# Kernel tuning notes

Hardware: AMD Instinct MI355X
Metric: run time of the kernel (lower is better)

Reference implementation:

```python
import jax, jax.numpy as jnp
import numpy as np

GAMMA = 0.9          # EMA momentum for prototype update
N_CLASSES = 201      # 200 classes + 1 background
K_PROTO = 5          # prototypes per class
FG_THRESH = 0.5      # pca_fg_threshold
SK_EPS = 0.05        # sinkhorn temperature (SwAV-style)
SK_ITERS = 3         # sinkhorn iterations
PCA_ITERS = 10       # niter of torch.pca_lowrank


def _l2norm(x, axis=-1):
    return x / jnp.maximum(jnp.linalg.norm(x, axis=axis, keepdims=True), 1e-12)


def _pca_first_component(X, key):
    # Randomized power iteration for the top left singular vector of the
    # centered data (mirrors torch.pca_lowrank(X, q=1, center=True, niter=10)).
    Xc = X - X.mean(0, keepdims=True)            # [N, D]
    G = Xc.T @ Xc                                # [D, D]
    v = jax.random.normal(key, (X.shape[1],), X.dtype)
    v = v / jnp.linalg.norm(v)
    def body(v, _):
        v = G @ v
        return v / jnp.maximum(jnp.linalg.norm(v), 1e-12), None
    v, _ = jax.lax.scan(body, v, None, length=PCA_ITERS)
    u = Xc @ v                                   # [N]
    return u / jnp.maximum(jnp.linalg.norm(u), 1e-12)


def _masked_sinkhorn(logits, mask):
    # logits: [C, BN, K], mask: [C, BN] bool (rows belonging to class c).
    # Vectorized equivalent of the per-class sinkhorn_knopp(L_c): returns a
    # row-stochastic assignment on the masked rows, balanced over the K cols.
    tiny = 1e-9
    m = mask[..., None].astype(logits.dtype)     # [C, BN, 1]
    Q = jnp.exp(logits / SK_EPS) * m
    n_c = jnp.maximum(mask.sum(-1).astype(logits.dtype), 1.0)[:, None, None]
    K = Q.shape[-1]
    Q = Q / jnp.maximum(Q.sum((-2, -1), keepdims=True), tiny)
    for _ in range(SK_ITERS):
        Q = Q / jnp.maximum(Q.sum(-2, keepdims=True), tiny) / K   # balance cols
        Q = Q * m
        Q = Q / jnp.maximum(Q.sum(-1, keepdims=True), tiny) / n_c # balance rows
        Q = Q * m
    return Q * n_c  # each masked row sums to 1


def setup_inputs() -> dict:
    key = jax.random.key(0)
    k1, k2, k3 = jax.random.split(key, 3)
    B, n_patches, dim = 32, 1024, 768
    patch_tokens = jax.random.normal(k1, (B, n_patches, dim), jnp.float32)
    prototypes = 0.02 * jax.random.normal(k2, (N_CLASSES, K_PROTO, dim), jnp.float32)
    labels = jax.random.randint(k3, (B,), 0, 200).astype(jnp.int64)
    return {"patch_tokens": patch_tokens, "prototypes": prototypes, "labels": labels}


def reference(patch_tokens, prototypes, labels):
    B, n_patches, D = patch_tokens.shape

    pt_norm = _l2norm(patch_tokens)              # [B, N, D]
    proto_norm = _l2norm(prototypes)             # [C, K, D]
    # B n_patches dim, C K dim -> B n_patches C K
    logits = jnp.einsum('bnd,ckd->bnck', pt_norm, proto_norm)

    # ---- get_pseudo_patch_labels (PCA foreground extraction) ----
    X = patch_tokens.reshape(-1, D)
    U = _pca_first_component(X, jax.random.key(1))
    U_scaled = (U - U.min()) / (U.max() - U.min())
    fg = (U_scaled < FG_THRESH).reshape(B, n_patches)
    patch_labels = jnp.where(fg, labels[:, None], N_CLASSES - 1)  # [B, N] int

    # ---- update_prototypes, vectorized over the 201-class python loop ----
    pl_flat = patch_labels.reshape(-1)                            # [B*N]
    L = jnp.transpose(logits.reshape(-1, N_CLASSES, K_PROTO), (1, 0, 2))  # [C, BN, K]
    class_ids = jnp.arange(N_CLASSES)
    mask = pl_flat[None, :] == class_ids[:, None]                 # [C, BN]
    Q = _masked_sinkhorn(L, mask)                                 # [C, BN, K]
    # P_c_new = L_c_assignment.T @ I_c, batched over classes
    P_new = jnp.einsum('cnk,nd->ckd', Q, pt_norm.reshape(-1, D))  # [C, K, D]
    present = (labels[None, :] == class_ids[:, None]).any(-1)     # 'c in labels'
    ema = GAMMA * prototypes + (1.0 - GAMMA) * P_new              # momentum_update
    new_prototypes = jnp.where(present[:, None, None], ema, prototypes)

    image_prototype_logits = logits.max(1)        # [B, C, K]
    class_logits = image_prototype_logits.sum(-1) # [B, C]
    return class_logits, image_prototype_logits, new_prototypes
```

## Files before the change

### kernel.cpp

```cpp
#include <hip/hip_runtime.h>
#include <stdint.h>
#include <stddef.h>

#define DEV static __device__ __forceinline__

typedef __attribute__((ext_vector_type(8))) short bf16x8;
typedef __attribute__((ext_vector_type(4))) float f32x4;

DEV float bf2f(unsigned short u){ union{unsigned int i; float f;} v; v.i = ((unsigned int)u)<<16; return v.f; }
DEV unsigned short f2bf(float f){ union{float f; unsigned int i;} v; v.f=f; unsigned int i=v.i;
  return (unsigned short)((i + 0x7FFFu + ((i>>16)&1u)) >> 16); }
DEV unsigned int fenc(float x){ unsigned int i = __float_as_uint(x); return (i & 0x80000000u) ? ~i : (i | 0x80000000u); }
DEV float fdec(unsigned int e){ unsigned int i = (e & 0x80000000u) ? (e & 0x7FFFFFFFu) : ~e; return __uint_as_float(i); }

DEV float waveSum(float s){
  for (int m=32;m;m>>=1) s += __shfl_xor(s, m, 64);
  return s;
}

DEV float blockSum(float v, float* red){
  int t = threadIdx.x;
  red[t] = v; __syncthreads();
  for (int k=128;k>0;k>>=1){ if (t<k) red[t] += red[t+k]; __syncthreads(); }
  float r = red[0]; __syncthreads();
  return r;
}

DEV void gl16(const unsigned short* g, unsigned short* lds){
  __builtin_amdgcn_global_load_lds(
      (const __attribute__((address_space(1))) void*)g,
      (__attribute__((address_space(3))) void*)lds, 16, 0, 0);
}

DEV float erfinv_f(float x){
  float w = -log1pf(-__fmul_rn(x,x));
  float p;
  if (w < 5.0f){
    w = w - 2.5f;
    p = 2.81022636e-08f;
    p = 3.43273939e-07f + p*w;
    p = -3.5233877e-06f + p*w;
    p = -4.39150654e-06f + p*w;
    p = 0.00021858087f + p*w;
    p = -0.00125372503f + p*w;
    p = -0.00417768164f + p*w;
    p = 0.246640727f + p*w;
    p = 1.50140941f + p*w;
  } else {
    w = sqrtf(w) - 3.0f;
    p = -0.000200214257f;
    p = 0.000100950558f + p*w;
    p = 0.00134934322f + p*w;
    p = -0.00367342844f + p*w;
    p = 0.00573950773f + p*w;
    p = -0.0076224613f + p*w;
    p = 0.00943887047f + p*w;
    p = 1.00167406f + p*w;
    p = 2.83297682f + p*w;
  }
  return p*x;
}

#define BN_TOT 32768
#define DIM 768
#define NCLS 201
#define KP 5
#define CKPAD 1024
#define GSPLIT 32
#define PSPLIT 8
#define LPAD 40


__global__ void k_setup(unsigned int* ipl_enc, int* cnt, int* cur, int* present,
                        unsigned int* minmax, float* meansum,
                        const int* __restrict__ raw, int* __restrict__ lab,
                        float* __restrict__ v){
  int i = blockIdx.x*256 + threadIdx.x;
  ipl_enc[i] = 0u;
  if (i < NCLS){ cnt[i]=0; cur[i]=0; present[i]=0; }
  if (i < DIM) meansum[i] = 0.f;
  if (i == 0){
    minmax[0]=0xFFFFFFFFu; minmax[1]=0u;
    bool is64 = true;
    for (int j=0;j<8;j++){
      int lo = raw[2*j], hi = raw[2*j+1];
      if (hi != 0 || lo < 0 || lo >= NCLS-1){ is64 = false; break; }
    }
    for (int j=0;j<32;j++) lab[j] = is64 ? raw[2*j] : raw[j];
  }
  if (i < DIM){
    unsigned int ks[3] = {0u, 1u, 0x1BD11BDBu};
    const int rot0[4] = {13,15,26,6};
    const int rot1[4] = {17,29,16,24};
    unsigned int x0 = 0u, x1 = (unsigned int)i;
    x0 += ks[0]; x1 += ks[1];
    #pragma unroll
    for (int g=0; g<5; g++){
      const int* rr = (g&1) ? rot1 : rot0;
      #pragma unroll
      for (int j=0;j<4;j++){
        x0 += x1;
        x1 = (x1 << rr[j]) | (x1 >> (32-rr[j]));
        x1 ^= x0;
      }
      x0 += ks[(g+1)%3];
      x1 += ks[(g+2)%3] + (unsigned int)(g+1);
    }
    unsigned int b = x0 ^ x1;
    const float lo = __uint_as_float(0xBF7FFFFFu);
    const float sq2 = __uint_as_float(0x3FB504F3u);
    float f = __uint_as_float((b>>9) | 0x3F800000u) - 1.0f;
    float uu = __fadd_rn(__fmul_rn(f, 2.0f), lo);
    uu = fmaxf(lo, uu);
    v[i] = sq2 * erfinv_f(uu);
  }
}

__global__ void k_proto(const float* __restrict__ protos, unsigned short* __restrict__ protn){
  int row = blockIdx.x;
  int l = threadIdx.x;
  if (row >= NCLS*KP){
    for (int j=0;j<12;j++) protn[(size_t)row*DIM + l + j*64] = 0;
    return;
  }
  const float* p = protos + (size_t)row*DIM;
  float x[12]; float s = 0.f;
  for (int j=0;j<12;j++){ x[j] = p[l + j*64]; s += x[j]*x[j]; }
  s = waveSum(s);
  float inv = 1.0f / fmaxf(sqrtf(s), 1e-12f);
  for (int j=0;j<12;j++) protn[(size_t)row*DIM + l + j*64] = f2bf(x[j]*inv);
}

__global__ void k_trans(const float* __restrict__ X, unsigned short* __restrict__ hiT,
                        unsigned short* __restrict__ loT, float* __restrict__ meansum){
  __shared__ float tile[64][65];
  __shared__ float colsum[4][64];
  int n0 = blockIdx.x*64, c0 = blockIdx.y*64;
  int t = threadIdx.x;
  float part = 0.f;
  for (int i=0;i<16;i++){
    int idx = t + i*256; int r = idx>>6, c = idx&63;
    float x = X[(size_t)(n0+r)*DIM + c0+c];
    tile[r][c] = x;
    part += x;
  }
  colsum[t>>6][t&63] = part;
  __syncthreads();
  for (int i=0;i<16;i++){
    int idx = t + i*256; int c = idx>>6, n = idx&63;
    float x = tile[n][c];
    unsigned short h = f2bf(x);
    float hf = bf2f(h);
    unsigned short lo = f2bf(x - hf);
    size_t o = (size_t)(c0+c)*BN_TOT + n0+n;
    hiT[o] = h; loT[o] = lo;
  }
  if (t < 64){
    float s = colsum[0][t]+colsum[1][t]+colsum[2][t]+colsum[3][t];
    atomicAdd(&meansum[c0+t], s);
  }
}

__global__ void k_ptn(const float* __restrict__ X, unsigned short* __restrict__ ptn){
  int row = blockIdx.x*4 + (threadIdx.x>>6);
  int l = threadIdx.x & 63;
  const float* p = X + (size_t)row*DIM;
  float x[12]; float s = 0.f;
  for (int j=0;j<12;j++){ x[j] = p[l + j*64]; s += x[j]*x[j]; }
  s = waveSum(s);
  float inv = 1.0f / fmaxf(sqrtf(s), 1e-12f);
  for (int j=0;j<12;j++) ptn[(size_t)row*DIM + l + j*64] = f2bf(x[j]*inv);
}

__global__ __launch_bounds__(256) void k_gemm_logits(const unsigned short* __restrict__ A,
                                                     const unsigned short* __restrict__ Bt,
                                                     unsigned int* __restrict__ ipl_enc){
  __shared__ __align__(16) unsigned short As[128][LPAD];
  __shared__ __align__(16) unsigned short Bs[128][LPAD];
  __shared__ float red[2][2][64];
  int flat = blockIdx.y*8 + blockIdx.x;
  int xcd = flat & 7, j = flat >> 3;
  int mb = xcd*32 + (j>>3);
  int nb = j & 7;
  int t = threadIdx.x;
  int w = t>>6, l = t&63;
  int wr = w>>1, wc = w&1;
  f32x4 acc[4][4];
  #pragma unroll
  for (int m=0;m<4;m++)
    #pragma unroll
    for (int n=0;n<4;n++){ acc[m][n][0]=0.f; acc[m][n][1]=0.f; acc[m][n][2]=0.f; acc[m][n][3]=0.f; }

  for (int kt=0; kt<24; kt++){
    int k0 = kt*32;
    __syncthreads();
    #pragma unroll
    for (int i=0;i<2;i++){
      int ch = t + i*256;
      int r = ch>>2, co = (ch&3)*8;
      *(uint4*)&As[r][co] = *(const uint4*)&A[(size_t)(mb*128 + r)*DIM + k0 + co];
      *(uint4*)&Bs[r][co] = *(const uint4*)&Bt[(size_t)(nb*128 + r)*DIM + k0 + co];
    }
    __syncthreads();
    bf16x8 a[4], b[4];
    #pragma unroll
    for (int m=0;m<4;m++) a[m] = *(const bf16x8*)&As[wr*64 + m*16 + (l&15)][(l>>4)*8];
    #pragma unroll
    for (int n=0;n<4;n++) b[n] = *(const bf16x8*)&Bs[wc*64 + n*16 + (l&15)][(l>>4)*8];
    #pragma unroll
    for (int m=0;m<4;m++)
      #pragma unroll
      for (int n=0;n<4;n++)
        acc[m][n] = __builtin_amdgcn_mfma_f32_16x16x32_bf16(a[m], b[n], acc[m][n], 0,0,0);
  }
  float vmax[4];
  #pragma unroll
  for (int n=0;n<4;n++){
    float v = -1e30f;
    #pragma unroll
    for (int m=0;m<4;m++)
      #pragma unroll
      for (int r=0;r<4;r++) v = fmaxf(v, acc[m][n][r]);
    v = fmaxf(v, __shfl_xor(v, 16, 64));
    v = fmaxf(v, __shfl_xor(v, 32, 64));
    vmax[n] = v;
  }
  __syncthreads();
  if (l < 16){
    #pragma unroll
    for (int n=0;n<4;n++) red[wc][wr][n*16 + l] = vmax[n];
  }
  __syncthreads();
  if (t < 128){
    int wcc = t>>6, col = t&63;
    float v = fmaxf(red[wcc][0][col], red[wcc][1][col]);
    int gcol = nb*128 + wcc*64 + col;
    if (gcol < NCLS*KP){
      int b = (mb*128) >> 10;
      atomicMax(&ipl_enc[b*CKPAD + gcol], fenc(v));
    }
  }
}

__global__ __launch_bounds__(256,2) void k_gemm_G(const unsigned short* __restrict__ hiT,
                                                  const unsigned short* __restrict__ loT,
                                                  float* __restrict__ Gpart){
  __shared__ __align__(16) unsigned short Ahi[2][128*32];
  __shared__ __align__(16) unsigned short Alo[2][128*32];
  __shared__ __align__(16) unsigned short Bhi[2][128*32];
  __shared__ __align__(16) unsigned short Blo[2][128*32];
  int b = blockIdx.x;
  int xcd = b & 7, q = b >> 3;
  int s = xcd + 8*(q/21);
  int p = q % 21;
  int ib = 0, rem = p;
  while (rem >= 6 - ib){ rem -= 6 - ib; ib++; }
  int jb = ib + rem;
  int t = threadIdx.x, w = t>>6, l = t&63;
  int wr = w>>1, wc = w&1;

  int gu = (l&3) ^ ((l>>2)&3) ^ ((l>>4)&3);
  size_t lane_off = (size_t)(l>>2)*BN_TOT + (size_t)gu*8;
  size_t baseA = (size_t)(ib*128)*BN_TOT;
  size_t baseB = (size_t)(jb*128)*BN_TOT;

  int physc = (l>>4) ^ (l&3) ^ ((l>>2)&3);
  int rdA = (wr*64 + (l&15))*32 + physc*8;
  int rdB = (wc*64 + (l&15))*32 + physc*8;

  f32x4 acc[4][4];
  #pragma unroll
  for (int m=0;m<4;m++)
    #pragma unroll
    for (int n=0;n<4;n++){ acc[m][n][0]=0.f; acc[m][n][1]=0.f; acc[m][n][2]=0.f; acc[m][n][3]=0.f; }

  #define STAGE_G(KT, SET) { \
    size_t k0 = (size_t)s*1024 + (size_t)(KT)*32; \
    _Pragma("unroll") \
    for (int ci=0; ci<2; ci++){ \
      int c = w + ci*4; \
      size_t roff = (size_t)(c*16)*BN_TOT + k0 + lane_off; \
      gl16(hiT + baseA + roff, &Ahi[SET][c*512]); \
      gl16(loT + baseA + roff, &Alo[SET][c*512]); \
      gl16(hiT + baseB + roff, &Bhi[SET][c*512]); \
      gl16(loT + baseB + roff, &Blo[SET][c*512]); \
    } }

  STAGE_G(0, 0);
  for (int kt=0; kt<32; kt++){
    int cur = kt & 1;
    if (kt+1 < 32){
      STAGE_G(kt+1, cur^1);
      asm volatile("s_waitcnt vmcnt(8)" ::: "memory");
    } else {
      asm volatile("s_waitcnt vmcnt(0)" ::: "memory");
    }
    __builtin_amdgcn_s_barrier();
    __builtin_amdgcn_sched_barrier(0);
    bf16x8 bh[4], bl[4];
    #pragma unroll
    for (int n=0;n<4;n++){
      bh[n] = *(const bf16x8*)&Bhi[cur][rdB + n*512];
      bl[n] = *(const bf16x8*)&Blo[cur][rdB + n*512];
    }
    #pragma unroll
    for (int m=0;m<4;m++){
      bf16x8 ah = *(const bf16x8*)&Ahi[cur][rdA + m*512];
      bf16x8 al = *(const bf16x8*)&Alo[cur][rdA + m*512];
      #pragma unroll
      for (int n=0;n<4;n++){
        acc[m][n] = __builtin_amdgcn_mfma_f32_16x16x32_bf16(ah, bh[n], acc[m][n], 0,0,0);
        acc[m][n] = __builtin_amdgcn_mfma_f32_16x16x32_bf16(ah, bl[n], acc[m][n], 0,0,0);
        acc[m][n] = __builtin_amdgcn_mfma_f32_16x16x32_bf16(al, bh[n], acc[m][n], 0,0,0);
      }
    }
    __builtin_amdgcn_s_barrier();
  }
  #undef STAGE_G

  float* out = Gpart + (size_t)s*DIM*DIM;
  #pragma unroll
  for (int m=0;m<4;m++)
    #pragma unroll
    for (int n=0;n<4;n++)
      #pragma unroll
      for (int r=0;r<4;r++){
        int row = ib*128 + wr*64 + m*16 + (l>>4)*4 + r;
        int col = jb*128 + wc*64 + n*16 + (l&15);
        out[(size_t)row*DIM + col] = acc[m][n][r];
        if (ib != jb) out[(size_t)col*DIM + row] = acc[m][n][r];
      }
}

__global__ void k_gfix(const float* __restrict__ Gpart, const float* __restrict__ meansum,
                       float* __restrict__ G){
  int i = blockIdx.x*256 + threadIdx.x;
  int r = i/DIM, c = i%DIM;
  float s = 0.f;
  for (int p=0;p<GSPLIT;p++) s += Gpart[(size_t)p*DIM*DIM + i];
  const float invN = 1.0f/32768.0f;
  float mr = meansum[r]*invN, mc = meansum[c]*invN;
  G[i] = s*invN - mr*mc;
}

__global__ void k_mv(const float* __restrict__ G, const float* __restrict__ vin,
                     float* __restrict__ vout){
  __shared__ float vs[DIM];
  int t = threadIdx.x;
  for (int i=t;i<DIM;i+=256) vs[i] = vin[i];
  __syncthreads();
  int row = blockIdx.x*4 + (t>>6), l = t&63;
  const float* g = G + (size_t)row*DIM;
  float s = 0.f;
  for (int j=0;j<12;j++) s += g[l + j*64]*vs[l + j*64];
  s = waveSum(s);
  if (l==0) vout[row] = s;
}

__global__ void k_muv(const float* __restrict__ meansum, const float* __restrict__ v,
                      float* __restrict__ scal){
  __shared__ float red[256];
  int t = threadIdx.x;
  float s = 0.f;
  for (int i=t;i<DIM;i+=256) s += meansum[i]*(1.0f/32768.0f)*v[i];
  float r = blockSum(s, red);
  if (t==0) scal[0] = r;
}

__global__ void k_u(const unsigned short* __restrict__ hiT, const unsigned short* __restrict__ loT,
                    const float* __restrict__ v, const float* __restrict__ scal,
                    float* __restrict__ u, unsigned int* __restrict__ minmax){
  __shared__ float vs[DIM];
  int t = threadIdx.x;
  for (int i=t;i<DIM;i+=256) vs[i] = v[i];
  __syncthreads();
  size_t n = (size_t)blockIdx.x*256 + t;
  float acc = 0.f;
  for (int c=0;c<DIM;c++){
    size_t o = (size_t)c*BN_TOT + n;
    acc += (bf2f(hiT[o]) + bf2f(loT[o])) * vs[c];
  }
  float val = acc - scal[0];
  u[n] = val;
  float mn = val, mx = val;
  for (int m=32;m;m>>=1){
    mn = fminf(mn, __shfl_xor(mn, m, 64));
    mx = fmaxf(mx, __shfl_xor(mx, m, 64));
  }
  __shared__ float smn[4], smx[4];
  int w = t>>6;
  if ((t&63)==0){ smn[w]=mn; smx[w]=mx; }
  __syncthreads();
  if (t==0){
    for (int k=1;k<4;k++){ mn = fminf(mn, smn[k]); mx = fmaxf(mx, smx[k]); }
    atomicMin(&minmax[0], fenc(mn));
    atomicMax(&minmax[1], fenc(mx));
  }
}

__global__ void k_pl(const float* __restrict__ u, const int* __restrict__ labels,
                     const unsigned int* __restrict__ minmax, int* __restrict__ pl,
                     int* __restrict__ cnt){
  int n = blockIdx.x*256 + threadIdx.x;
  float umin = fdec(minmax[0]), umax = fdec(minmax[1]);
  float us = (u[n]-umin)/(umax-umin);
  int c = (us < 0.5f) ? labels[n>>10] : (NCLS-1);
  pl[n] = c;
  if (c < NCLS-1) atomicAdd(&cnt[c], 1);
}

__global__ void k_offs(const int* __restrict__ cnt, int* __restrict__ offs,
                       const int* __restrict__ labels, int* __restrict__ present){
  if (threadIdx.x == 0){
    int acc = 0;
    for (int c=0;c<NCLS-1;c++){ offs[c] = acc; acc += cnt[c]; }
    offs[NCLS-1] = acc;
  }
  if (threadIdx.x < 32) atomicOr(&present[labels[threadIdx.x]], 1);
}

__global__ void k_scatter(const int* __restrict__ pl, const int* __restrict__ offs,
                          int* __restrict__ cur, int* __restrict__ idx){
  int n = blockIdx.x*256 + threadIdx.x;
  int c = pl[n];
  if (c < NCLS-1){
    int p = offs[c] + atomicAdd(&cur[c], 1);
    idx[p] = n;
  }
}

__global__ void k_qlog(const int* __restrict__ idx, const int* __restrict__ offs,
                       const int* __restrict__ pl, const unsigned short* __restrict__ ptn,
                       const unsigned short* __restrict__ protn, float* __restrict__ q){
  int i = blockIdx.x*4 + (threadIdx.x>>6);
  int l = threadIdx.x & 63;
  int total = offs[NCLS-1];
  if (i >= total) return;
  int n = idx[i];
  int c = pl[n];
  const unsigned short* pr = ptn + (size_t)n*DIM;
  float x[12];
  for (int j=0;j<12;j++) x[j] = bf2f(pr[l + j*64]);
  for (int k=0;k<KP;k++){
    const unsigned short* wv = protn + (size_t)(c*KP + k)*DIM;
    float s = 0.f;
    for (int j=0;j<12;j++) s += x[j]*bf2f(wv[l + j*64]);
    s = waveSum(s);
    if (l==0) q[(size_t)i*KP + k] = expf(s*20.0f);
  }
}

__global__ void k_sink(const int* __restrict__ cnt, const int* __restrict__ offs,
                       float* __restrict__ q){
  __shared__ float red[256];
  __shared__ float colf[KP];
  int c = blockIdx.x;
  int nc = cnt[c];
  if (nc == 0) return;
  int n0 = offs[c];
  float* Q = q + (size_t)n0*KP;
  int t = threadIdx.x;
  int tot5 = nc*KP;
  float s = 0.f;
  for (int i=t;i<tot5;i+=256) s += Q[i];
  float total = blockSum(s, red);
  float sc = 1.0f/fmaxf(total, 1e-9f);
  for (int i=t;i<tot5;i+=256) Q[i] *= sc;
  __syncthreads();
  float ncf = (float)nc;
  for (int it=0; it<3; it++){
    float cs[KP] = {0,0,0,0,0};
    for (int i=t;i<nc;i+=256){
      const float* row = Q + (size_t)i*KP;
      #pragma unroll
      for (int k=0;k<KP;k++) cs[k] += row[k];
    }
    for (int k=0;k<KP;k++){
      float v = blockSum(cs[k], red);
      if (t==0) colf[k] = 1.0f/(fmaxf(v,1e-9f)*(float)KP);
    }
    __syncthreads();
    for (int i=t;i<nc;i+=256){
      float* row = Q + (size_t)i*KP;
      float qq[KP]; float rs = 0.f;
      #pragma unroll
      for (int k=0;k<KP;k++){ qq[k] = row[k]*colf[k]; rs += qq[k]; }
      float rf = 1.0f/(fmaxf(rs,1e-9f)*ncf);
      #pragma unroll
      for (int k=0;k<KP;k++) row[k] = qq[k]*rf;
    }
    __syncthreads();
  }
  for (int i=t;i<tot5;i+=256) Q[i] *= ncf;
}

__global__ void k_pnew(const int* __restrict__ cnt, const int* __restrict__ offs,
                       const int* __restrict__ present, const int* __restrict__ idx,
                       const float* __restrict__ q, const unsigned short* __restrict__ ptn,
                       float* __restrict__ P4){
  int c = blockIdx.y, s = blockIdx.x;
  if (!present[c]) return;
  int nc = cnt[c], n0 = offs[c];
  int r0 = n0 + (nc*s)/PSPLIT;
  int r1 = n0 + (nc*(s+1))/PSPLIT;
  int t = threadIdx.x;
  float acc[KP][3];
  #pragma unroll
  for (int k=0;k<KP;k++){ acc[k][0]=0.f; acc[k][1]=0.f; acc[k][2]=0.f; }
  for (int i=r0; i<r1; ++i){
    int n = idx[i];
    float qv[KP];
    #pragma unroll
    for (int k=0;k<KP;k++) qv[k] = q[(size_t)i*KP + k];
    const unsigned short* row = ptn + (size_t)n*DIM;
    #pragma unroll
    for (int j=0;j<3;j++){
      float x = bf2f(row[t + j*256]);
      #pragma unroll
      for (int k=0;k<KP;k++) acc[k][j] += qv[k]*x;
    }
  }
  float* out = P4 + ((size_t)(s*NCLS + c)*KP)*DIM;
  #pragma unroll
  for (int k=0;k<KP;k++)
    #pragma unroll
    for (int j=0;j<3;j++)
      out[(size_t)k*DIM + t + j*256] = acc[k][j];
}

__global__ void k_ema(const float* __restrict__ protos, const float* __restrict__ P4,
                      const int* __restrict__ present, float* __restrict__ out){
  int i = blockIdx.x*256 + threadIdx.x;
  if (i >= NCLS*KP*DIM) return;
  int c = i / (KP*DIM);
  float p = protos[i];
  if (present[c]){
    float s = 0.f;
    #pragma unroll
    for (int sp=0; sp<PSPLIT; sp++) s += P4[(size_t)sp*NCLS*KP*DIM + i];
    out[i] = 0.9f*p + 0.1f*s;
  } else {
    out[i] = p;
  }
}

__global__ void k_final(const unsigned int* __restrict__ ipl_enc, float* __restrict__ out){
  int i = blockIdx.x*256 + threadIdx.x;
  if (i < 32*NCLS*KP){
    int b = i / (NCLS*KP), ck = i % (NCLS*KP);
    out[32*NCLS + i] = fdec(ipl_enc[b*CKPAD + ck]);
  }
  if (i < 32*NCLS){
    int b = i / NCLS, c = i % NCLS;
    float s = 0.f;
    #pragma unroll
    for (int k=0;k<KP;k++) s += fdec(ipl_enc[b*CKPAD + c*KP + k]);
    out[b*NCLS + c] = s;
  }
}

extern "C" void kernel_launch(void* const* d_in, const int* in_sizes, int n_in,
                              void* d_out, int out_size, void* d_ws, size_t ws_size,
                              hipStream_t stream){
  (void)in_sizes; (void)n_in; (void)out_size; (void)ws_size;
  const float* X = (const float*)d_in[0];
  const float* protos = (const float*)d_in[1];
  const int* labels_raw = (const int*)d_in[2];
  float* out = (float*)d_out;

  char* w = (char*)d_ws;
  size_t off = 0;
  auto alloc = [&](size_t bytes)->void*{
    void* p = (void*)(w + off);
    off = (off + bytes + 255) & ~(size_t)255;
    return p;
  };
  unsigned short* hiT   = (unsigned short*)alloc((size_t)DIM*BN_TOT*2);
  unsigned short* loT   = (unsigned short*)alloc((size_t)DIM*BN_TOT*2);
  unsigned short* ptn   = (unsigned short*)alloc((size_t)BN_TOT*DIM*2);
  unsigned short* protn = (unsigned short*)alloc((size_t)CKPAD*DIM*2);
  float* Gpart   = (float*)alloc((size_t)GSPLIT*DIM*DIM*4);
  float* G       = (float*)alloc((size_t)DIM*DIM*4);
  float* meansum = (float*)alloc(DIM*4);
  float* vA      = (float*)alloc(DIM*4);
  float* vB      = (float*)alloc(DIM*4);
  float* scal    = (float*)alloc(256);
  int* cnt       = (int*)alloc(1024);
  int* cur       = (int*)alloc(1024);
  int* offs      = (int*)alloc(1024);
  int* present   = (int*)alloc(1024);
  int* labc      = (int*)alloc(256);
  unsigned int* minmax  = (unsigned int*)alloc(256);
  unsigned int* ipl_enc = (unsigned int*)alloc((size_t)32*CKPAD*4);

  char* gb = (char*)Gpart;
  size_t goff = 0;
  auto galloc = [&](size_t bytes)->void*{
    void* p = (void*)(gb + goff);
    goff = (goff + bytes + 255) & ~(size_t)255;
    return p;
  };
  float* u_  = (float*)galloc(BN_TOT*4);
  int* pl_   = (int*)galloc(BN_TOT*4);
  int* idx_  = (int*)galloc(BN_TOT*4);
  float* q_  = (float*)galloc((size_t)BN_TOT*KP*4);
  float* P4_ = (float*)galloc((size_t)PSPLIT*NCLS*KP*DIM*4);

  dim3 b256(256);
  k_setup<<<dim3(128), b256, 0, stream>>>(ipl_enc, cnt, cur, present, minmax, meansum,
                                          labels_raw, labc, vA);
  k_proto<<<dim3(CKPAD), dim3(64), 0, stream>>>(protos, protn);
  k_trans<<<dim3(512,12), b256, 0, stream>>>(X, hiT, loT, meansum);
  k_ptn<<<dim3(8192), b256, 0, stream>>>(X, ptn);
  k_gemm_logits<<<dim3(8,256), b256, 0, stream>>>(ptn, protn, ipl_enc);
  k_gemm_G<<<dim3(21*GSPLIT), b256, 0, stream>>>(hiT, loT, Gpart);
  k_gfix<<<dim3(2304), b256, 0, stream>>>(Gpart, meansum, G);
  for (int it=0; it<10; it++){
    float* src = (it&1) ? vB : vA;
    float* dst = (it&1) ? vA : vB;
    k_mv<<<dim3(192), b256, 0, stream>>>(G, src, dst);
  }
  k_muv<<<dim3(1), b256, 0, stream>>>(meansum, vA, scal);
  k_u<<<dim3(128), b256, 0, stream>>>(hiT, loT, vA, scal, u_, minmax);
  k_pl<<<dim3(128), b256, 0, stream>>>(u_, labc, minmax, pl_, cnt);
  k_offs<<<dim3(1), b256, 0, stream>>>(cnt, offs, labc, present);
  k_scatter<<<dim3(128), b256, 0, stream>>>(pl_, offs, cur, idx_);
  k_qlog<<<dim3(8192), b256, 0, stream>>>(idx_, offs, pl_, ptn, protn, q_);
  k_sink<<<dim3(200), b256, 0, stream>>>(cnt, offs, q_);
  k_pnew<<<dim3(PSPLIT,NCLS), b256, 0, stream>>>(cnt, offs, present, idx_, q_, ptn, P4_);
  k_ema<<<dim3(3015), b256, 0, stream>>>(protos, P4_, present, out + 32*NCLS + 32*NCLS*KP);
  k_final<<<dim3(126), b256, 0, stream>>>(ipl_enc, out);
}
```

Measured before the change: 526.6 us.

## Single-buffer G GEMM, symmetric-read gfix, and row-parallel u projection from fp32 X

The Gram GEMM drops its LDS double-buffered pipeline for a single buffer guarded by two syncthreads per k-step and changes the swizzle term. It also stops writing the mirrored lower triangle, and k_gfix now reads the upper-triangle tile instead. The u = Xc·v projection now reads the original fp32 X row-wise with one wave per row across 2048 blocks, replacing the strided column walk over hi/lo bf16 transposes in 128 blocks. This aims to cut redundant stores and to give the projection coalesced access with more parallelism, at the risk of losing load/compute overlap in the GEMM.

```diff
diff --git a/kernel.cpp b/kernel.cpp
--- a/kernel.cpp
+++ b/kernel.cpp
@@ -242,13 +242,13 @@
   }
 }
 
-__global__ __launch_bounds__(256,2) void k_gemm_G(const unsigned short* __restrict__ hiT,
-                                                  const unsigned short* __restrict__ loT,
-                                                  float* __restrict__ Gpart){
-  __shared__ __align__(16) unsigned short Ahi[2][128*32];
-  __shared__ __align__(16) unsigned short Alo[2][128*32];
-  __shared__ __align__(16) unsigned short Bhi[2][128*32];
-  __shared__ __align__(16) unsigned short Blo[2][128*32];
+__global__ __launch_bounds__(256) void k_gemm_G(const unsigned short* __restrict__ hiT,
+                                                const unsigned short* __restrict__ loT,
+                                                float* __restrict__ Gpart){
+  __shared__ __align__(16) unsigned short Ahi[128*32];
+  __shared__ __align__(16) unsigned short Alo[128*32];
+  __shared__ __align__(16) unsigned short Bhi[128*32];
+  __shared__ __align__(16) unsigned short Blo[128*32];
   int b = blockIdx.x;
   int xcd = b & 7, q = b >> 3;
   int s = xcd + 8*(q/21);
@@ -259,7 +259,7 @@
   int t = threadIdx.x, w = t>>6, l = t&63;
   int wr = w>>1, wc = w&1;
 
-  int gu = (l&3) ^ ((l>>2)&3) ^ ((l>>4)&3);
+  int gu = (l&3) ^ ((l>>2)&3) ^ (l>>4);
   size_t lane_off = (size_t)(l>>2)*BN_TOT + (size_t)gu*8;
   size_t baseA = (size_t)(ib*128)*BN_TOT;
   size_t baseB = (size_t)(jb*128)*BN_TOT;
@@ -274,39 +274,29 @@
     #pragma unroll
     for (int n=0;n<4;n++){ acc[m][n][0]=0.f; acc[m][n][1]=0.f; acc[m][n][2]=0.f; acc[m][n][3]=0.f; }
 
-  #define STAGE_G(KT, SET) { \
-    size_t k0 = (size_t)s*1024 + (size_t)(KT)*32; \
-    _Pragma("unroll") \
-    for (int ci=0; ci<2; ci++){ \
-      int c = w + ci*4; \
-      size_t roff = (size_t)(c*16)*BN_TOT + k0 + lane_off; \
-      gl16(hiT + baseA + roff, &Ahi[SET][c*512]); \
-      gl16(loT + baseA + roff, &Alo[SET][c*512]); \
-      gl16(hiT + baseB + roff, &Bhi[SET][c*512]); \
-      gl16(loT + baseB + roff, &Blo[SET][c*512]); \
-    } }
-
-  STAGE_G(0, 0);
   for (int kt=0; kt<32; kt++){
-    int cur = kt & 1;
-    if (kt+1 < 32){
-      STAGE_G(kt+1, cur^1);
-      asm volatile("s_waitcnt vmcnt(8)" ::: "memory");
-    } else {
-      asm volatile("s_waitcnt vmcnt(0)" ::: "memory");
-    }
-    __builtin_amdgcn_s_barrier();
-    __builtin_amdgcn_sched_barrier(0);
+    size_t k0 = (size_t)s*1024 + (size_t)kt*32;
+    __syncthreads();
+    #pragma unroll
+    for (int ci=0; ci<2; ci++){
+      int c = w + ci*4;
+      size_t roff = (size_t)(c*16)*BN_TOT + k0 + lane_off;
+      gl16(hiT + baseA + roff, &Ahi[c*512]);
+      gl16(loT + baseA + roff, &Alo[c*512]);
+      gl16(hiT + baseB + roff, &Bhi[c*512]);
+      gl16(loT + baseB + roff, &Blo[c*512]);
+    }
+    __syncthreads();
     bf16x8 bh[4], bl[4];
     #pragma unroll
     for (int n=0;n<4;n++){
-      bh[n] = *(const bf16x8*)&Bhi[cur][rdB + n*512];
-      bl[n] = *(const bf16x8*)&Blo[cur][rdB + n*512];
+      bh[n] = *(const bf16x8*)&Bhi[rdB + n*512];
+      bl[n] = *(const bf16x8*)&Blo[rdB + n*512];
     }
     #pragma unroll
     for (int m=0;m<4;m++){
-      bf16x8 ah = *(const bf16x8*)&Ahi[cur][rdA + m*512];
-      bf16x8 al = *(const bf16x8*)&Alo[cur][rdA + m*512];
+      bf16x8 ah = *(const bf16x8*)&Ahi[rdA + m*512];
+      bf16x8 al = *(const bf16x8*)&Alo[rdA + m*512];
       #pragma unroll
       for (int n=0;n<4;n++){
         acc[m][n] = __builtin_amdgcn_mfma_f32_16x16x32_bf16(ah, bh[n], acc[m][n], 0,0,0);
@@ -314,9 +304,7 @@
         acc[m][n] = __builtin_amdgcn_mfma_f32_16x16x32_bf16(al, bh[n], acc[m][n], 0,0,0);
       }
     }
-    __builtin_amdgcn_s_barrier();
-  }
-  #undef STAGE_G
+  }
 
   float* out = Gpart + (size_t)s*DIM*DIM;
   #pragma unroll
@@ -328,7 +316,6 @@
         int row = ib*128 + wr*64 + m*16 + (l>>4)*4 + r;
         int col = jb*128 + wc*64 + n*16 + (l&15);
         out[(size_t)row*DIM + col] = acc[m][n][r];
-        if (ib != jb) out[(size_t)col*DIM + row] = acc[m][n][r];
       }
 }
 
@@ -336,8 +323,11 @@
                        float* __restrict__ G){
   int i = blockIdx.x*256 + threadIdx.x;
   int r = i/DIM, c = i%DIM;
+  int rt = r>>7, ct = c>>7;
+  int rr = (rt<=ct) ? r : c, cc = (rt<=ct) ? c : r;
+  size_t o = (size_t)rr*DIM + cc;
   float s = 0.f;
-  for (int p=0;p<GSPLIT;p++) s += Gpart[(size_t)p*DIM*DIM + i];
+  for (int p=0;p<GSPLIT;p++) s += Gpart[(size_t)p*DIM*DIM + o];
   const float invN = 1.0f/32768.0f;
   float mr = meansum[r]*invN, mc = meansum[c]*invN;
   G[i] = s*invN - mr*mc;
@@ -367,29 +357,35 @@
   if (t==0) scal[0] = r;
 }
 
-__global__ void k_u(const unsigned short* __restrict__ hiT, const unsigned short* __restrict__ loT,
-                    const float* __restrict__ v, const float* __restrict__ scal,
+__global__ void k_u(const float* __restrict__ X, const float* __restrict__ v,
+                    const float* __restrict__ scal,
                     float* __restrict__ u, unsigned int* __restrict__ minmax){
   __shared__ float vs[DIM];
+  __shared__ float smn[4], smx[4];
   int t = threadIdx.x;
   for (int i=t;i<DIM;i+=256) vs[i] = v[i];
   __syncthreads();
-  size_t n = (size_t)blockIdx.x*256 + t;
-  float acc = 0.f;
-  for (int c=0;c<DIM;c++){
-    size_t o = (size_t)c*BN_TOT + n;
-    acc += (bf2f(hiT[o]) + bf2f(loT[o])) * vs[c];
-  }
-  float val = acc - scal[0];
-  u[n] = val;
-  float mn = val, mx = val;
-  for (int m=32;m;m>>=1){
-    mn = fminf(mn, __shfl_xor(mn, m, 64));
-    mx = fmaxf(mx, __shfl_xor(mx, m, 64));
-  }
-  __shared__ float smn[4], smx[4];
-  int w = t>>6;
-  if ((t&63)==0){ smn[w]=mn; smx[w]=mx; }
+  int w = t>>6, l = t&63;
+  float mn = 1e30f, mx = -1e30f;
+  #pragma unroll
+  for (int rr=0; rr<4; rr++){
+    int row = blockIdx.x*16 + w*4 + rr;
+    const float4* xr = (const float4*)(X + (size_t)row*DIM);
+    float s = 0.f;
+    #pragma unroll
+    for (int j=0;j<3;j++){
+      float4 x4 = xr[l + j*64];
+      int base = 4*(l + j*64);
+      s += x4.x*vs[base] + x4.y*vs[base+1] + x4.z*vs[base+2] + x4.w*vs[base+3];
+    }
+    s = waveSum(s);
+    if (l==0){
+      float val = s - scal[0];
+      u[row] = val;
+      mn = fminf(mn, val); mx = fmaxf(mx, val);
+    }
+  }
+  if (l==0){ smn[w]=mn; smx[w]=mx; }
   __syncthreads();
   if (t==0){
     for (int k=1;k<4;k++){ mn = fminf(mn, smn[k]); mx = fmaxf(mx, smx[k]); }
@@ -621,7 +617,7 @@
     k_mv<<<dim3(192), b256, 0, stream>>>(G, src, dst);
   }
   k_muv<<<dim3(1), b256, 0, stream>>>(meansum, vA, scal);
-  k_u<<<dim3(128), b256, 0, stream>>>(hiT, loT, vA, scal, u_, minmax);
+  k_u<<<dim3(2048), b256, 0, stream>>>(X, vA, scal, u_, minmax);
   k_pl<<<dim3(128), b256, 0, stream>>>(u_, labc, minmax, pl_, cnt);
   k_offs<<<dim3(1), b256, 0, stream>>>(cnt, offs, labc, present);
   k_scatter<<<dim3(128), b256, 0, stream>>>(pl_, offs, cur, idx_);
```

Measured after the change: 557.3 us. 5.8% more time.
